# Kernel optimization log

Hardware: AMD Instinct MI355X
Metric: run time of the kernel (lower is better)

Reference implementation:

```python
import jax, jax.numpy as jnp
import numpy as np

B, A, C, M, E = 8, 100000, 8, 128, 32
ALPHA, GAMMA = 0.25, 2.0


def setup_inputs() -> dict:
    key = jax.random.key(0)
    k1, k2, k3, k4, k5, k6, k7 = jax.random.split(key, 7)
    classifications = jax.random.uniform(k1, (B, A, C), dtype=jnp.float32)
    regressions = jax.random.normal(k2, (B, A, 8), dtype=jnp.float32)
    embeddings = jax.random.normal(k3, (B, A, E), dtype=jnp.float32)
    # anchors: random centers on a 1920x1080 image, reasonable w/h -> x1,y1,x2,y2
    cx = jax.random.uniform(k4, (A,), minval=0.0, maxval=1920.0)
    cy = jax.random.uniform(jax.random.fold_in(k4, 1), (A,), minval=0.0, maxval=1080.0)
    w = jax.random.uniform(jax.random.fold_in(k4, 2), (A,), minval=16.0, maxval=256.0)
    h = jax.random.uniform(jax.random.fold_in(k4, 3), (A,), minval=16.0, maxval=256.0)
    anchors = jnp.stack([cx - 0.5 * w, cy - 0.5 * h, cx + 0.5 * w, cy + 0.5 * h], axis=1)[None].astype(jnp.float32)
    # annotations: 16 coords = jittered 3D-box corner projections around a random box,
    # col 16 = object id, col 17 = class label in [0, C)
    bcx = jax.random.uniform(k5, (B, M, 1), minval=100.0, maxval=1820.0)
    bcy = jax.random.uniform(jax.random.fold_in(k5, 1), (B, M, 1), minval=100.0, maxval=980.0)
    bw = jax.random.uniform(jax.random.fold_in(k5, 2), (B, M, 1), minval=30.0, maxval=300.0)
    bh = jax.random.uniform(jax.random.fold_in(k5, 3), (B, M, 1), minval=30.0, maxval=300.0)
    jit = jax.random.uniform(k6, (B, M, 16), minval=-0.4, maxval=0.4)
    sx = jnp.array([-1, -1, 1, 1, -1, -1, 1, 1], jnp.float32)
    sy = jnp.array([-1, 1, -1, 1, -1, 1, -1, 1], jnp.float32)
    xs = bcx + 0.5 * bw * (sx + jit[..., 0:16:2])
    ys = bcy + 0.5 * bh * (sy + jit[..., 1:16:2])
    coords = jnp.stack([xs, ys], axis=-1).reshape(B, M, 16)
    ids = jax.random.randint(k7, (B, M, 1), 0, 1000).astype(jnp.float32)
    cls_lab = jax.random.randint(jax.random.fold_in(k7, 1), (B, M, 1), 0, C).astype(jnp.float32)
    annotations = jnp.concatenate([coords, ids, cls_lab], axis=-1)
    return {
        "classifications": classifications,
        "regressions": regressions,
        "anchors": anchors,
        "annotations": annotations,
        "embeddings": embeddings,
    }


def calc_iou(a, b):
    # a: [A,4], b: [M,4] in x1,y1,x2,y2 -> [A,M]
    area = (b[:, 2] - b[:, 0]) * (b[:, 3] - b[:, 1])
    iw = jnp.minimum(a[:, 2:3], b[None, :, 2]) - jnp.maximum(a[:, 0:1], b[None, :, 0])
    ih = jnp.minimum(a[:, 3:4], b[None, :, 3]) - jnp.maximum(a[:, 1:2], b[None, :, 1])
    iw = jnp.clip(iw, 0.0)
    ih = jnp.clip(ih, 0.0)
    ua = ((a[:, 2] - a[:, 0]) * (a[:, 3] - a[:, 1]))[:, None] + area[None, :] - iw * ih
    return iw * ih / jnp.clip(ua, 1e-8)


_S2 = jnp.array([-1, -1, 1, 1, -1, -1, 1, 1], jnp.float32)
_S4 = jnp.array([-1, 1, -1, 1, -1, 1, -1, 1], jnp.float32)
_S6 = jnp.array([1, 1, 1, 1, -1, -1, -1, -1], jnp.float32)


def _per_image(cls, reg, ann, anchor):
    # cls [A,C], reg [A,8], ann [M,18], anchor [A,4]
    aw = anchor[:, 2] - anchor[:, 0]
    ah = anchor[:, 3] - anchor[:, 1]
    acx = anchor[:, 0] + 0.5 * aw
    acy = anchor[:, 1] + 0.5 * ah
    cls = jnp.clip(cls, 1e-4, 1.0 - 1e-4)
    valid = ann[:, -1] >= 0.0  # [M]; annotations with class -1 are padding
    xs, ys = ann[:, 0:16:2], ann[:, 1:16:2]
    box2d = jnp.stack([xs.min(1), ys.min(1), xs.max(1), ys.max(1)], axis=1)  # [M,4]
    iou = jnp.where(valid[None, :], calc_iou(anchor, box2d), -1.0)  # [A,M]
    iou_max = iou.max(1)
    assigned = ann[iou.argmax(1)]  # [A,18]
    pos = iou_max >= 0.5
    neg = iou_max < 0.4
    num_pos = jnp.maximum(pos.sum().astype(cls.dtype), 1.0)

    onehot = jax.nn.one_hot(assigned[:, -1].astype(jnp.int32), cls.shape[1], dtype=cls.dtype)
    targets = jnp.where(pos[:, None], onehot, jnp.where(neg[:, None], 0.0, -1.0))
    alpha_f = jnp.where(targets == 1.0, ALPHA, 1.0 - ALPHA)
    focal_w = alpha_f * jnp.where(targets == 1.0, 1.0 - cls, cls) ** GAMMA
    bce = -(targets * jnp.log(cls) + (1.0 - targets) * jnp.log(1.0 - cls))
    cls_loss = jnp.where(targets != -1.0, focal_w * bce, 0.0).sum() / num_pos

    t = assigned[:, :16]

    def vp(rx, ry, tx, ty):
        denom = jnp.sqrt(rx * rx + ry * ry) * jnp.sqrt(tx * tx + ty * ty)
        return 1.0 - (rx * tx + ry * ty) / jnp.maximum(denom, 1e-8)

    vp1 = vp(reg[:, 2], reg[:, 3],
             (t[:, 4] + t[:, 6] + t[:, 12] + t[:, 14] - (t[:, 0] + t[:, 2] + t[:, 8] + t[:, 10])) / 4.0,
             (t[:, 5] + t[:, 7] + t[:, 13] + t[:, 15] - (t[:, 1] + t[:, 3] + t[:, 9] + t[:, 11])) / 4.0)
    vp2 = vp(reg[:, 4], reg[:, 5],
             (t[:, 2] + t[:, 6] + t[:, 10] + t[:, 14] - (t[:, 0] + t[:, 4] + t[:, 8] + t[:, 12])) / 4.0,
             (t[:, 3] + t[:, 7] + t[:, 11] + t[:, 15] - (t[:, 1] + t[:, 5] + t[:, 9] + t[:, 13])) / 4.0)
    vp3 = vp(reg[:, 6], reg[:, 7],
             (t[:, 0] + t[:, 2] + t[:, 4] + t[:, 6] - (t[:, 8] + t[:, 10] + t[:, 12] + t[:, 14])) / 4.0,
             (t[:, 1] + t[:, 3] + t[:, 5] + t[:, 7] - (t[:, 9] + t[:, 11] + t[:, 13] + t[:, 15])) / 4.0)
    vp_all = (vp1 + vp2 + vp3) / 3.0
    vp_loss = (vp_all * pos).sum() / num_pos

    # corner predictions from (ctr_x, ctr_y, v1, v2, v3) offsets: [A,8] x-coords, [A,8] y-coords
    px = reg[:, 0:1] + reg[:, 2:3] * _S2 + reg[:, 4:5] * _S4 + reg[:, 6:7] * _S6
    py = reg[:, 1:2] + reg[:, 3:4] * _S2 + reg[:, 5:6] * _S4 + reg[:, 7:8] * _S6
    tx = (t[:, 0:16:2] - acx[:, None]) / aw[:, None]
    ty = (t[:, 1:16:2] - acy[:, None]) / ah[:, None]
    diff = jnp.concatenate([jnp.abs(px - tx), jnp.abs(py - ty)], axis=1)  # [A,16]
    sl1 = jnp.where(diff <= 1.0 / 9.0, 0.5 * 9.0 * diff * diff, diff - 0.5 / 9.0)
    reg_loss = (sl1.mean(1) * pos).sum() / num_pos
    return cls_loss, reg_loss, vp_loss


def reference(classifications, regressions, anchors, annotations, embeddings):
    anchor = anchors[0]
    cls_l, reg_l, vp_l = jax.vmap(_per_image, in_axes=(0, 0, 0, None))(
        classifications, regressions, annotations, anchor)
    return jnp.stack([cls_l.mean(), reg_l.mean(), vp_l.mean()])


if __name__ == "__main__":
    print(reference(**setup_inputs()))
```

## Files before the change

kernel.cpp:

```cpp
#include <hip/hip_runtime.h>

namespace {

constexpr int B_N = 8;
constexpr int A_N = 100000;
constexpr int M_N = 128;
constexpr int BLOCK = 256;
constexpr int NBLK = (A_N + BLOCK - 1) / BLOCK;
constexpr int GX = 16, GY = 9, NC = GX * GY;
constexpr float CELL = 120.0f;
constexpr float MARGIN = 128.0f;

constexpr size_t OFF_BOX  = 0;
constexpr size_t OFF_MASK = OFF_BOX + (size_t)B_N * M_N * 8 * 4;
constexpr size_t OFF_PART = OFF_MASK + (size_t)B_N * NC * 2 * 8;

__global__ void k0_prep(const float* __restrict__ ann_, float* __restrict__ boxbuf)
{
    const int i = blockIdx.x * blockDim.x + threadIdx.x;
    if (i >= B_N * M_N) return;
    const float* t = ann_ + (size_t)i * 18;
    float minx = t[0], maxx = t[0], miny = t[1], maxy = t[1];
#pragma unroll
    for (int j = 1; j < 8; ++j) {
        const float xj = t[2 * j], yj = t[2 * j + 1];
        minx = fminf(minx, xj); maxx = fmaxf(maxx, xj);
        miny = fminf(miny, yj); maxy = fmaxf(maxy, yj);
    }
    float area = (maxx - minx) * (maxy - miny);
    if (t[17] < 0.0f) {
        minx = 1e30f; miny = 1e30f; maxx = -1e30f; maxy = -1e30f; area = 0.0f;
    }
    float* o = boxbuf + (size_t)i * 8;
    o[0] = minx; o[1] = miny; o[2] = maxx; o[3] = maxy;
    o[4] = area; o[5] = 0.f;  o[6] = 0.f;  o[7] = 0.f;
}

__global__ void kmask(const float* __restrict__ boxbuf,
                      unsigned long long* __restrict__ maskbuf)
{
    const int cell = blockIdx.x, b = blockIdx.y, m = threadIdx.x;
    const int cx = cell % GX, cy = cell / GX;
    const float lox = cx * CELL - MARGIN, hix = cx * CELL + CELL + MARGIN;
    const float loy = cy * CELL - MARGIN, hiy = cy * CELL + CELL + MARGIN;
    const float* r = boxbuf + ((size_t)b * M_N + m) * 8;
    const bool ok = (r[0] <= hix) && (r[2] >= lox) && (r[1] <= hiy) && (r[3] >= loy);
    const unsigned long long bal = __ballot(ok);
    if ((m & 63) == 0)
        maskbuf[((size_t)b * NC + cell) * 2 + (m >> 6)] = bal;
}

__global__ __launch_bounds__(BLOCK) void ka_fused(
    const float* __restrict__ cls_,
    const float* __restrict__ reg_,
    const float* __restrict__ anchors_,
    const float* __restrict__ ann_,
    const float* __restrict__ boxbuf,
    const unsigned* __restrict__ maskbuf,
    float* __restrict__ partials)
{
    __shared__ float s_x1[M_N], s_y1[M_N], s_x2[M_N], s_y2[M_N], s_nb[M_N];
    __shared__ unsigned s_mask[NC * 4];

    const int b = blockIdx.y, blk = blockIdx.x, tid = threadIdx.x;

    if (tid < M_N) {
        const float* r = boxbuf + ((size_t)b * M_N + tid) * 8;
        s_x1[tid] = r[0]; s_y1[tid] = r[1];
        s_x2[tid] = r[2]; s_y2[tid] = r[3];
        s_nb[tid] = -r[4];
    }
    for (int i = tid; i < NC * 4; i += BLOCK)
        s_mask[i] = maskbuf[(size_t)b * NC * 4 + i];
    __syncthreads();

    const int a  = blk * BLOCK + tid;
    const int ca = min(a, A_N - 1);
    const float4 an = ((const float4*)anchors_)[ca];
    const float* cp = cls_ + ((size_t)b * A_N + ca) * 8;
    const float4 cA = ((const float4*)cp)[0];
    const float4 cB = ((const float4*)cp)[1];

    const float aarea = (an.z - an.x) * (an.w - an.y);
    const float acx = 0.5f * (an.x + an.z);
    const float acy = 0.5f * (an.y + an.w);
    const int cellx = min(GX - 1, max(0, (int)(acx * (1.0f / CELL))));
    const int celly = min(GY - 1, max(0, (int)(acy * (1.0f / CELL))));
    const int cell  = celly * GX + cellx;

    float m1 = -3e38f, m2 = -3e38f;
    float bn = 0.f, bs = 1.f;
    int   kb = 0;

#pragma unroll
    for (int q = 0; q < 4; ++q) {
        unsigned w = s_mask[cell * 4 + q];
        while (__any(w != 0u)) {
            const bool have = (w != 0u);
            const int  bit  = __ffs(w) - 1;
            const int  m    = q * 32 + (have ? bit : 0);
            w &= w - 1;
            const float x1 = s_x1[m], y1 = s_y1[m];
            const float x2 = s_x2[m], y2 = s_y2[m];
            const float nbر = s_nb[m];
            const float nb = have ? nbر : -3e37f;
            const float iw = fminf(an.z, x2) - fmaxf(an.x, x1);
            const float ih = fminf(an.w, y2) - fmaxf(an.y, y1);
            const float in_raw = fmaxf(iw, 0.f) * fmaxf(ih, 0.f);
            const float in_ = have ? in_raw : 0.f;
            const float t1 = __builtin_fmaf(3.0f, in_, nb);
            const float t2 = __builtin_fmaf(3.5f, in_, nb);
            m1 = fmaxf(m1, t1);
            m2 = fmaxf(m2, t2);
            const float s = aarea - nb;
            const bool  u = (in_ * bs > bn * s);
            bn = u ? in_ : bn;
            bs = u ? s   : bs;
            kb = u ? m   : kb;
        }
    }

    const bool inb = (a < A_N);
    const bool pos = inb && (m1 >= aarea);
    const bool nonign = pos || (m2 < aarea);

    float clsS = 0.f, regS = 0.f, vpS = 0.f, posC = 0.f;

    const float pv[8] = {cA.x, cA.y, cA.z, cA.w, cB.x, cB.y, cB.z, cB.w};
    {
        float s = 0.f;
#pragma unroll
        for (int c = 0; c < 8; ++c) {
            const float p = fminf(fmaxf(pv[c], 1e-4f), 1.0f - 1e-4f);
            s += 0.75f * p * p * (-__logf(1.0f - p));
        }
        clsS = (inb && nonign) ? s : 0.f;
    }

    if (pos) {
        posC = 1.0f;
        const float* t = ann_ + ((size_t)b * M_N + kb) * 18;
        float tt[16];
#pragma unroll
        for (int j = 0; j < 16; ++j) tt[j] = t[j];
        const int kc = (int)t[17];

        float pkc = 0.5f;
#pragma unroll
        for (int c = 0; c < 8; ++c)
            if (c == kc) pkc = fminf(fmaxf(pv[c], 1e-4f), 1.0f - 1e-4f);
        const float negkc   = 0.75f * pkc * pkc * (-__logf(1.0f - pkc));
        const float posterm = 0.25f * (1.0f - pkc) * (1.0f - pkc) * (-__logf(pkc));
        clsS += posterm - negkc;

        const float aw = an.z - an.x;
        const float ah = an.w - an.y;
        const float* rp = reg_ + ((size_t)b * A_N + a) * 8;
        const float4 r0 = ((const float4*)rp)[0];
        const float4 r1 = ((const float4*)rp)[1];

        auto vp = [](float rx, float ry, float tx, float ty) {
            const float denom = sqrtf(rx * rx + ry * ry) * sqrtf(tx * tx + ty * ty);
            return 1.0f - (rx * tx + ry * ty) / fmaxf(denom, 1e-8f);
        };
        const float vp1 = vp(r0.z, r0.w,
            (tt[4] + tt[6] + tt[12] + tt[14] - (tt[0] + tt[2] + tt[8] + tt[10])) * 0.25f,
            (tt[5] + tt[7] + tt[13] + tt[15] - (tt[1] + tt[3] + tt[9] + tt[11])) * 0.25f);
        const float vp2 = vp(r1.x, r1.y,
            (tt[2] + tt[6] + tt[10] + tt[14] - (tt[0] + tt[4] + tt[8] + tt[12])) * 0.25f,
            (tt[3] + tt[7] + tt[11] + tt[15] - (tt[1] + tt[5] + tt[9] + tt[13])) * 0.25f);
        const float vp3 = vp(r1.z, r1.w,
            (tt[0] + tt[2] + tt[4] + tt[6] - (tt[8] + tt[10] + tt[12] + tt[14])) * 0.25f,
            (tt[1] + tt[3] + tt[5] + tt[7] - (tt[9] + tt[11] + tt[13] + tt[15])) * 0.25f);
        vpS = (vp1 + vp2 + vp3) * (1.0f / 3.0f);

        const float s2[8] = {-1, -1, 1, 1, -1, -1, 1, 1};
        const float s4[8] = {-1, 1, -1, 1, -1, 1, -1, 1};
        const float s6[8] = {1, 1, 1, 1, -1, -1, -1, -1};
        const float acx2 = an.x + 0.5f * aw;
        const float acy2 = an.y + 0.5f * ah;
        float ssum = 0.f;
#pragma unroll
        for (int j = 0; j < 8; ++j) {
            const float px = r0.x + r0.z * s2[j] + r1.x * s4[j] + r1.z * s6[j];
            const float py = r0.y + r0.w * s2[j] + r1.y * s4[j] + r1.w * s6[j];
            const float tx = (tt[2 * j]     - acx2) / aw;
            const float ty = (tt[2 * j + 1] - acy2) / ah;
            const float dx = fabsf(px - tx);
            const float dy = fabsf(py - ty);
            ssum += (dx <= (1.0f / 9.0f)) ? 4.5f * dx * dx : dx - (0.5f / 9.0f);
            ssum += (dy <= (1.0f / 9.0f)) ? 4.5f * dy * dy : dy - (0.5f / 9.0f);
        }
        regS = ssum * (1.0f / 16.0f);
    }

#pragma unroll
    for (int off = 32; off; off >>= 1) {
        clsS += __shfl_down(clsS, off);
        regS += __shfl_down(regS, off);
        vpS  += __shfl_down(vpS, off);
        posC += __shfl_down(posC, off);
    }
    __shared__ float s_red[4][4];
    const int wv = tid >> 6, ln = tid & 63;
    if (ln == 0) {
        s_red[wv][0] = clsS; s_red[wv][1] = regS;
        s_red[wv][2] = vpS;  s_red[wv][3] = posC;
    }
    __syncthreads();
    if (tid == 0) {
        float C = 0, R = 0, V = 0, P = 0;
        for (int w2 = 0; w2 < 4; ++w2) {
            C += s_red[w2][0]; R += s_red[w2][1];
            V += s_red[w2][2]; P += s_red[w2][3];
        }
        float* out = partials + ((size_t)b * NBLK + blk) * 4;
        out[0] = C; out[1] = R; out[2] = V; out[3] = P;
    }
}

__global__ __launch_bounds__(BLOCK) void kc_final(
    const float* __restrict__ partials,
    float* __restrict__ out)
{
    const int tid = threadIdx.x;
    __shared__ float s[4][4];
    __shared__ float accum[3];
    if (tid == 0) { accum[0] = 0.f; accum[1] = 0.f; accum[2] = 0.f; }

    for (int b = 0; b < B_N; ++b) {
        float c = 0.f, r = 0.f, v = 0.f, p = 0.f;
        for (int i = tid; i < NBLK; i += BLOCK) {
            const float* q = partials + ((size_t)b * NBLK + i) * 4;
            c += q[0]; r += q[1]; v += q[2]; p += q[3];
        }
#pragma unroll
        for (int off = 32; off; off >>= 1) {
            c += __shfl_down(c, off); r += __shfl_down(r, off);
            v += __shfl_down(v, off); p += __shfl_down(p, off);
        }
        const int wv = tid >> 6, ln = tid & 63;
        if (ln == 0) { s[wv][0] = c; s[wv][1] = r; s[wv][2] = v; s[wv][3] = p; }
        __syncthreads();
        if (tid == 0) {
            float C = 0, R = 0, V = 0, P = 0;
            for (int w = 0; w < 4; ++w) {
                C += s[w][0]; R += s[w][1]; V += s[w][2]; P += s[w][3];
            }
            const float np_ = fmaxf(P, 1.0f);
            accum[0] += C / np_; accum[1] += R / np_; accum[2] += V / np_;
        }
        __syncthreads();
    }
    if (tid == 0) {
        out[0] = accum[0] * 0.125f;
        out[1] = accum[1] * 0.125f;
        out[2] = accum[2] * 0.125f;
    }
}

}

extern "C" void kernel_launch(void* const* d_in, const int* in_sizes, int n_in,
                              void* d_out, int out_size, void* d_ws, size_t ws_size,
                              hipStream_t stream)
{
    const float* cls_    = (const float*)d_in[0];
    const float* reg_    = (const float*)d_in[1];
    const float* anchors = (const float*)d_in[2];
    const float* ann     = (const float*)d_in[3];

    char* ws = (char*)d_ws;
    float*              boxbuf  = (float*)(ws + OFF_BOX);
    unsigned long long* maskbuf = (unsigned long long*)(ws + OFF_MASK);
    float*              partials = (float*)(ws + OFF_PART);

    k0_prep<<<dim3((B_N * M_N + BLOCK - 1) / BLOCK), dim3(BLOCK), 0, stream>>>(ann, boxbuf);
    kmask<<<dim3(NC, B_N), dim3(M_N), 0, stream>>>(boxbuf, maskbuf);
    ka_fused<<<dim3(NBLK, B_N), dim3(BLOCK), 0, stream>>>(
        cls_, reg_, anchors, ann, boxbuf, (const unsigned*)maskbuf, partials);
    kc_final<<<dim3(1), dim3(BLOCK), 0, stream>>>(partials, (float*)d_out);
}
```

Baseline: 65.11 us.

## Bucket anchors by grid cell so each block shares one compacted box list

Adds histogram, scan and scatter kernels that sort anchors by spatial grid cell. The main kernel then gives each block the anchors of a single cell and loops uniformly over a compacted list of candidate boxes held in shared memory. This removes the per-lane bitmask walk and the wave divergence that came from anchors in different cells. Annotations are also staged in shared memory. The cost is three extra launches, a serial single-block scan over 391 blocks, gather-style loads of cls/reg through sidx, and a fixed CPC=6 chunks per cell. If a cell holds more than 1536 anchors, the extra anchors are silently dropped.

```diff
diff --git a/kernel.cpp b/kernel.cpp
--- a/kernel.cpp
+++ b/kernel.cpp
@@ -6,14 +6,29 @@
 constexpr int A_N = 100000;
 constexpr int M_N = 128;
 constexpr int BLOCK = 256;
-constexpr int NBLK = (A_N + BLOCK - 1) / BLOCK;
+constexpr int NBLK_S = (A_N + BLOCK - 1) / BLOCK;
 constexpr int GX = 16, GY = 9, NC = GX * GY;
 constexpr float CELL = 120.0f;
 constexpr float MARGIN = 128.0f;
+constexpr int CPC = 6;
+constexpr int NCH = NC * CPC;
 
 constexpr size_t OFF_BOX  = 0;
 constexpr size_t OFF_MASK = OFF_BOX + (size_t)B_N * M_N * 8 * 4;
-constexpr size_t OFF_PART = OFF_MASK + (size_t)B_N * NC * 2 * 8;
+constexpr size_t OFF_HIST = OFF_MASK + (size_t)B_N * NC * 2 * 8;
+constexpr size_t OFF_OFFS = OFF_HIST + (size_t)NBLK_S * NC * 4;
+constexpr size_t OFF_CB   = OFF_OFFS + (size_t)NC * NBLK_S * 4;
+constexpr size_t OFF_SIDX = (OFF_CB + (NC + 1) * 4 + 15) & ~size_t(15);
+constexpr size_t OFF_SANC = (OFF_SIDX + (size_t)A_N * 4 + 15) & ~size_t(15);
+constexpr size_t OFF_PART = OFF_SANC + (size_t)A_N * 16;
+
+__device__ __forceinline__ int cell_of(const float4& an) {
+    const float acx = 0.5f * (an.x + an.z);
+    const float acy = 0.5f * (an.y + an.w);
+    const int cx = min(GX - 1, max(0, (int)(acx * (1.0f / CELL))));
+    const int cy = min(GY - 1, max(0, (int)(acy * (1.0f / CELL))));
+    return cy * GX + cx;
+}
 
 __global__ void k0_prep(const float* __restrict__ ann_, float* __restrict__ boxbuf)
 {
@@ -50,82 +65,157 @@
         maskbuf[((size_t)b * NC + cell) * 2 + (m >> 6)] = bal;
 }
 
-__global__ __launch_bounds__(BLOCK) void ka_fused(
+__global__ __launch_bounds__(BLOCK) void s1_hist(
+    const float* __restrict__ anchors_, unsigned* __restrict__ hist)
+{
+    __shared__ unsigned h[NC];
+    const int tid = threadIdx.x, blk = blockIdx.x;
+    for (int i = tid; i < NC; i += BLOCK) h[i] = 0u;
+    __syncthreads();
+    const int a = blk * BLOCK + tid;
+    if (a < A_N) {
+        const float4 an = ((const float4*)anchors_)[a];
+        atomicAdd(&h[cell_of(an)], 1u);
+    }
+    __syncthreads();
+    for (int i = tid; i < NC; i += BLOCK) hist[(size_t)blk * NC + i] = h[i];
+}
+
+__global__ __launch_bounds__(BLOCK) void s2_scan(
+    const unsigned* __restrict__ hist,
+    unsigned* __restrict__ offs, unsigned* __restrict__ cellBase)
+{
+    __shared__ unsigned tot[NC];
+    const int t = threadIdx.x;
+    if (t < NC) {
+        unsigned run = 0;
+        for (int k = 0; k < NBLK_S; ++k) {
+            offs[(size_t)t * NBLK_S + k] = run;
+            run += hist[(size_t)k * NC + t];
+        }
+        tot[t] = run;
+    }
+    __syncthreads();
+    if (t == 0) {
+        unsigned run = 0;
+        for (int c = 0; c < NC; ++c) { cellBase[c] = run; run += tot[c]; }
+        cellBase[NC] = run;
+    }
+}
+
+__global__ __launch_bounds__(BLOCK) void s3_scatter(
+    const float* __restrict__ anchors_,
+    const unsigned* __restrict__ offs, const unsigned* __restrict__ cellBase,
+    unsigned* __restrict__ sidx, float4* __restrict__ sanc)
+{
+    __shared__ int cellArr[BLOCK];
+    const int tid = threadIdx.x, blk = blockIdx.x;
+    const int a = blk * BLOCK + tid;
+    const bool v = (a < A_N);
+    float4 an = make_float4(0.f, 0.f, 0.f, 0.f);
+    int c = -1;
+    if (v) { an = ((const float4*)anchors_)[a]; c = cell_of(an); }
+    cellArr[tid] = c;
+    __syncthreads();
+    if (v) {
+        int rank = 0;
+        for (int j = 0; j < tid; ++j) rank += (cellArr[j] == c);
+        const unsigned d = cellBase[c] + offs[(size_t)c * NBLK_S + blk] + (unsigned)rank;
+        sidx[d] = (unsigned)a;
+        sanc[d] = an;
+    }
+}
+
+__global__ __launch_bounds__(BLOCK) void ka2(
     const float* __restrict__ cls_,
     const float* __restrict__ reg_,
-    const float* __restrict__ anchors_,
     const float* __restrict__ ann_,
     const float* __restrict__ boxbuf,
     const unsigned* __restrict__ maskbuf,
+    const unsigned* __restrict__ cellBase,
+    const unsigned* __restrict__ sidx,
+    const float4* __restrict__ sanc,
     float* __restrict__ partials)
 {
+    const int cc = blockIdx.x / CPC, chunk = blockIdx.x % CPC;
+    const int b = blockIdx.y, tid = threadIdx.x;
+    const int base = (int)cellBase[cc];
+    const int n    = (int)cellBase[cc + 1] - base;
+
+    if (chunk * BLOCK >= n) {
+        if (tid == 0) {
+            float* o = partials + ((size_t)b * NCH + blockIdx.x) * 4;
+            o[0] = 0.f; o[1] = 0.f; o[2] = 0.f; o[3] = 0.f;
+        }
+        return;
+    }
+
     __shared__ float s_x1[M_N], s_y1[M_N], s_x2[M_N], s_y2[M_N], s_nb[M_N];
-    __shared__ unsigned s_mask[NC * 4];
-
-    const int b = blockIdx.y, blk = blockIdx.x, tid = threadIdx.x;
-
+    __shared__ int   s_id[M_N];
+    __shared__ unsigned s_mask[4], s_pre[4];
+    __shared__ int s_Kv;
+    __shared__ float s_ann[M_N * 18];
+
+    for (int i = tid; i < M_N * 18; i += BLOCK)
+        s_ann[i] = ann_[(size_t)b * M_N * 18 + i];
+    if (tid < 4) s_mask[tid] = maskbuf[((size_t)b * NC + cc) * 4 + tid];
+    __syncthreads();
+    if (tid == 0) {
+        unsigned p = 0;
+#pragma unroll
+        for (int w = 0; w < 4; ++w) { s_pre[w] = p; p += __popc(s_mask[w]); }
+        s_Kv = (int)p;
+    }
+    __syncthreads();
     if (tid < M_N) {
-        const float* r = boxbuf + ((size_t)b * M_N + tid) * 8;
-        s_x1[tid] = r[0]; s_y1[tid] = r[1];
-        s_x2[tid] = r[2]; s_y2[tid] = r[3];
-        s_nb[tid] = -r[4];
-    }
-    for (int i = tid; i < NC * 4; i += BLOCK)
-        s_mask[i] = maskbuf[(size_t)b * NC * 4 + i];
-    __syncthreads();
-
-    const int a  = blk * BLOCK + tid;
-    const int ca = min(a, A_N - 1);
-    const float4 an = ((const float4*)anchors_)[ca];
-    const float* cp = cls_ + ((size_t)b * A_N + ca) * 8;
+        const unsigned w = s_mask[tid >> 5];
+        if ((w >> (tid & 31)) & 1u) {
+            const int r = (int)(s_pre[tid >> 5] + __popc(w & ((1u << (tid & 31)) - 1u)));
+            const float* rec = boxbuf + ((size_t)b * M_N + tid) * 8;
+            s_x1[r] = rec[0]; s_y1[r] = rec[1];
+            s_x2[r] = rec[2]; s_y2[r] = rec[3];
+            s_nb[r] = -rec[4];
+            s_id[r] = tid;
+        }
+    }
+    __syncthreads();
+    const int K = s_Kv;
+
+    const int i0  = chunk * BLOCK + tid;
+    const bool inb = (i0 < n);
+    const int gi  = base + (inb ? i0 : 0);
+    const float4 an = sanc[gi];
+    const int a = (int)sidx[gi];
+
+    const float* cp = cls_ + ((size_t)b * A_N + a) * 8;
     const float4 cA = ((const float4*)cp)[0];
     const float4 cB = ((const float4*)cp)[1];
 
     const float aarea = (an.z - an.x) * (an.w - an.y);
-    const float acx = 0.5f * (an.x + an.z);
-    const float acy = 0.5f * (an.y + an.w);
-    const int cellx = min(GX - 1, max(0, (int)(acx * (1.0f / CELL))));
-    const int celly = min(GY - 1, max(0, (int)(acy * (1.0f / CELL))));
-    const int cell  = celly * GX + cellx;
-
     float m1 = -3e38f, m2 = -3e38f;
     float bn = 0.f, bs = 1.f;
     int   kb = 0;
 
-#pragma unroll
-    for (int q = 0; q < 4; ++q) {
-        unsigned w = s_mask[cell * 4 + q];
-        while (__any(w != 0u)) {
-            const bool have = (w != 0u);
-            const int  bit  = __ffs(w) - 1;
-            const int  m    = q * 32 + (have ? bit : 0);
-            w &= w - 1;
-            const float x1 = s_x1[m], y1 = s_y1[m];
-            const float x2 = s_x2[m], y2 = s_y2[m];
-            const float nbر = s_nb[m];
-            const float nb = have ? nbر : -3e37f;
-            const float iw = fminf(an.z, x2) - fmaxf(an.x, x1);
-            const float ih = fminf(an.w, y2) - fmaxf(an.y, y1);
-            const float in_raw = fmaxf(iw, 0.f) * fmaxf(ih, 0.f);
-            const float in_ = have ? in_raw : 0.f;
-            const float t1 = __builtin_fmaf(3.0f, in_, nb);
-            const float t2 = __builtin_fmaf(3.5f, in_, nb);
-            m1 = fmaxf(m1, t1);
-            m2 = fmaxf(m2, t2);
-            const float s = aarea - nb;
-            const bool  u = (in_ * bs > bn * s);
-            bn = u ? in_ : bn;
-            bs = u ? s   : bs;
-            kb = u ? m   : kb;
-        }
-    }
-
-    const bool inb = (a < A_N);
+    for (int m = 0; m < K; ++m) {
+        const float x1 = s_x1[m], y1 = s_y1[m];
+        const float x2 = s_x2[m], y2 = s_y2[m];
+        const float nb = s_nb[m];
+        const float iw = fminf(an.z, x2) - fmaxf(an.x, x1);
+        const float ih = fminf(an.w, y2) - fmaxf(an.y, y1);
+        const float in_ = fmaxf(iw, 0.f) * fmaxf(ih, 0.f);
+        m1 = fmaxf(m1, __builtin_fmaf(3.0f, in_, nb));
+        m2 = fmaxf(m2, __builtin_fmaf(3.5f, in_, nb));
+        const float s = aarea - nb;
+        const bool  u = (in_ * bs > bn * s);
+        bn = u ? in_ : bn;
+        bs = u ? s   : bs;
+        kb = u ? m   : kb;
+    }
+
     const bool pos = inb && (m1 >= aarea);
     const bool nonign = pos || (m2 < aarea);
 
     float clsS = 0.f, regS = 0.f, vpS = 0.f, posC = 0.f;
-
     const float pv[8] = {cA.x, cA.y, cA.z, cA.w, cB.x, cB.y, cB.z, cB.w};
     {
         float s = 0.f;
@@ -139,7 +229,7 @@
 
     if (pos) {
         posC = 1.0f;
-        const float* t = ann_ + ((size_t)b * M_N + kb) * 18;
+        const float* t = s_ann + s_id[kb] * 18;
         float tt[16];
 #pragma unroll
         for (int j = 0; j < 16; ++j) tt[j] = t[j];
@@ -174,16 +264,16 @@
             (tt[1] + tt[3] + tt[5] + tt[7] - (tt[9] + tt[11] + tt[13] + tt[15])) * 0.25f);
         vpS = (vp1 + vp2 + vp3) * (1.0f / 3.0f);
 
-        const float s2[8] = {-1, -1, 1, 1, -1, -1, 1, 1};
-        const float s4[8] = {-1, 1, -1, 1, -1, 1, -1, 1};
-        const float s6[8] = {1, 1, 1, 1, -1, -1, -1, -1};
+        const float s2v[8] = {-1, -1, 1, 1, -1, -1, 1, 1};
+        const float s4v[8] = {-1, 1, -1, 1, -1, 1, -1, 1};
+        const float s6v[8] = {1, 1, 1, 1, -1, -1, -1, -1};
         const float acx2 = an.x + 0.5f * aw;
         const float acy2 = an.y + 0.5f * ah;
         float ssum = 0.f;
 #pragma unroll
         for (int j = 0; j < 8; ++j) {
-            const float px = r0.x + r0.z * s2[j] + r1.x * s4[j] + r1.z * s6[j];
-            const float py = r0.y + r0.w * s2[j] + r1.y * s4[j] + r1.w * s6[j];
+            const float px = r0.x + r0.z * s2v[j] + r1.x * s4v[j] + r1.z * s6v[j];
+            const float py = r0.y + r0.w * s2v[j] + r1.y * s4v[j] + r1.w * s6v[j];
             const float tx = (tt[2 * j]     - acx2) / aw;
             const float ty = (tt[2 * j + 1] - acy2) / ah;
             const float dx = fabsf(px - tx);
@@ -214,7 +304,7 @@
             C += s_red[w2][0]; R += s_red[w2][1];
             V += s_red[w2][2]; P += s_red[w2][3];
         }
-        float* out = partials + ((size_t)b * NBLK + blk) * 4;
+        float* out = partials + ((size_t)b * NCH + blockIdx.x) * 4;
         out[0] = C; out[1] = R; out[2] = V; out[3] = P;
     }
 }
@@ -230,8 +320,8 @@
 
     for (int b = 0; b < B_N; ++b) {
         float c = 0.f, r = 0.f, v = 0.f, p = 0.f;
-        for (int i = tid; i < NBLK; i += BLOCK) {
-            const float* q = partials + ((size_t)b * NBLK + i) * 4;
+        for (int i = tid; i < NCH; i += BLOCK) {
+            const float* q = partials + ((size_t)b * NCH + i) * 4;
             c += q[0]; r += q[1]; v += q[2]; p += q[3];
         }
 #pragma unroll
@@ -273,11 +363,21 @@
     char* ws = (char*)d_ws;
     float*              boxbuf  = (float*)(ws + OFF_BOX);
     unsigned long long* maskbuf = (unsigned long long*)(ws + OFF_MASK);
-    float*              partials = (float*)(ws + OFF_PART);
+    unsigned*           hist    = (unsigned*)(ws + OFF_HIST);
+    unsigned*           offs    = (unsigned*)(ws + OFF_OFFS);
+    unsigned*           cellBase= (unsigned*)(ws + OFF_CB);
+    unsigned*           sidxp   = (unsigned*)(ws + OFF_SIDX);
+    float4*             sancp   = (float4*)(ws + OFF_SANC);
+    float*              partials= (float*)(ws + OFF_PART);
 
     k0_prep<<<dim3((B_N * M_N + BLOCK - 1) / BLOCK), dim3(BLOCK), 0, stream>>>(ann, boxbuf);
     kmask<<<dim3(NC, B_N), dim3(M_N), 0, stream>>>(boxbuf, maskbuf);
-    ka_fused<<<dim3(NBLK, B_N), dim3(BLOCK), 0, stream>>>(
-        cls_, reg_, anchors, ann, boxbuf, (const unsigned*)maskbuf, partials);
+    s1_hist<<<dim3(NBLK_S), dim3(BLOCK), 0, stream>>>(anchors, hist);
+    s2_scan<<<dim3(1), dim3(BLOCK), 0, stream>>>(hist, offs, cellBase);
+    s3_scatter<<<dim3(NBLK_S), dim3(BLOCK), 0, stream>>>(anchors, offs, cellBase,
+                                                         sidxp, sancp);
+    ka2<<<dim3(NCH, B_N), dim3(BLOCK), 0, stream>>>(
+        cls_, reg_, ann, boxbuf, (const unsigned*)maskbuf, cellBase,
+        sidxp, sancp, partials);
     kc_final<<<dim3(1), dim3(BLOCK), 0, stream>>>(partials, (float*)d_out);
 }
```

Result: slower. 149.6 us (+129.7%).
